# Kernel tuning notes

Hardware: AMD Instinct MI355X
Metric: run time of the kernel (lower is better)

Reference implementation:

```python
import jax, jax.numpy as jnp
import numpy as np

N_NODES = 100000
N_EDGES = 3200000


def sage_conv(x, src, dst, Wl, bl, Wr, n_nodes):
    # PyG SAGEConv: out = lin_l(mean_{j in N(i)} x_j) + lin_r(x_i)
    msgs = x[src]                                            # [E, d]
    agg = jax.ops.segment_sum(msgs, dst, num_segments=n_nodes)
    cnt = jax.ops.segment_sum(jnp.ones((src.shape[0],), x.dtype), dst,
                              num_segments=n_nodes)
    mean = agg / jnp.maximum(cnt, 1.0)[:, None]
    return mean @ Wl.T + bl + x @ Wr.T


def setup_inputs() -> dict:
    key = jax.random.key(0)
    ks = jax.random.split(key, 9)
    x = jax.random.normal(ks[0], (N_NODES, 6), dtype=jnp.float32)
    edge_index = jax.random.randint(ks[1], (2, N_EDGES), 0, N_NODES, dtype=jnp.int32)
    def glorot(k, shape):
        fan_in = shape[1]
        return jax.random.normal(k, shape, dtype=jnp.float32) / np.sqrt(fan_in)
    return {
        "x": x,
        "edge_index": edge_index,
        "W1l": glorot(ks[2], (12, 6)), "b1": jnp.zeros((12,), jnp.float32),
        "W1r": glorot(ks[3], (12, 6)),
        "W2l": glorot(ks[4], (24, 12)), "b2": jnp.zeros((24,), jnp.float32),
        "W2r": glorot(ks[5], (24, 12)),
        "W3l": glorot(ks[6], (6, 24)), "b3": jnp.zeros((6,), jnp.float32),
        "W3r": glorot(ks[7], (6, 24)),
    }


def reference(x, edge_index, W1l, b1, W1r, W2l, b2, W2r, W3l, b3, W3r):
    src, dst = edge_index[0], edge_index[1]
    h = jax.nn.relu(sage_conv(x, src, dst, W1l, b1, W1r, N_NODES))
    h = jax.nn.relu(sage_conv(h, src, dst, W2l, b2, W2r, N_NODES))
    z = sage_conv(h, src, dst, W3l, b3, W3r, N_NODES)          # [N, 6] encoding
    return z
```

## Files before the change

kernel.cpp:

```cpp
#include <hip/hip_runtime.h>
#include <hip/hip_fp16.h>


#define BSHIFT 9
#define BMASK  511
#define NBMAX  256
#define PART_EDGES 4096
#define BCAP   18000

#define NTL(p) __builtin_nontemporal_load(p)

__device__ __forceinline__ unsigned h2u(__half2 h) { return *reinterpret_cast<unsigned*>(&h); }
__device__ __forceinline__ __half2 u2h(unsigned u) { return *reinterpret_cast<__half2*>(&u); }

__device__ __forceinline__ __half2 red32(__half2 v) {
    int x;
    x = __builtin_amdgcn_update_dpp(0, (int)h2u(v), 0x128, 0xf, 0xf, true);
    v = __hadd2(v, u2h((unsigned)x));
    x = __builtin_amdgcn_update_dpp(0, (int)h2u(v), 0x124, 0xf, 0xf, true);
    v = __hadd2(v, u2h((unsigned)x));
    x = __builtin_amdgcn_update_dpp(0, (int)h2u(v), 0x122, 0xf, 0xf, true);
    v = __hadd2(v, u2h((unsigned)x));
    x = __builtin_amdgcn_update_dpp(0, (int)h2u(v), 0x121, 0xf, 0xf, true);
    v = __hadd2(v, u2h((unsigned)x));
    v = __hadd2(v, u2h(__shfl_xor(h2u(v), 16, 64)));
    return v;
}

__device__ __forceinline__ int wscan_incl(int x) {
    x += __builtin_amdgcn_update_dpp(0, x, 0x111, 0xf, 0xf, true);
    x += __builtin_amdgcn_update_dpp(0, x, 0x112, 0xf, 0xf, true);
    x += __builtin_amdgcn_update_dpp(0, x, 0x114, 0xf, 0xf, true);
    x += __builtin_amdgcn_update_dpp(0, x, 0x118, 0xf, 0xf, true);
    x += __builtin_amdgcn_update_dpp(0, x, 0x142, 0xa, 0xf, true);
    x += __builtin_amdgcn_update_dpp(0, x, 0x143, 0xc, 0xf, true);
    return x;
}

__global__ void __launch_bounds__(256)
partition_kernel(const float* __restrict__ x, __half* __restrict__ xh,
                 __half* __restrict__ h1, __half* __restrict__ z3lh,
                 const int* __restrict__ src, const int* __restrict__ dst,
                 int* __restrict__ bcur, unsigned* __restrict__ pairs,
                 int E, int n, int nb) {
    __shared__ int hcnt[NBMAX];
    __shared__ int hbase[NBMAX];
    __shared__ int lofs[NBMAX];
    __shared__ int wtot[4];
    __shared__ unsigned sorted[PART_EDGES];
    __shared__ int gpos[PART_EDGES];

    int t = threadIdx.x;

    int gid = blockIdx.x * 256 + t;
    if (gid <= n) {
        uint4 o = make_uint4(0u, 0u, 0u, 0u);
        if (gid < n) {
            const float2* xp = reinterpret_cast<const float2*>(x + (size_t)gid * 6);
            float2 a = xp[0], b = xp[1], c = xp[2];
            o.x = h2u(__floats2half2_rn(a.x, a.y));
            o.y = h2u(__floats2half2_rn(b.x, b.y));
            o.z = h2u(__floats2half2_rn(c.x, c.y));
        }
        *reinterpret_cast<uint4*>(xh + (size_t)gid * 8) = o;
    }
    if (blockIdx.x == 0) {
        if (t < 16) h1[(size_t)n * 16 + t] = __float2half(0.f);
        if (t < 8)  z3lh[(size_t)n * 8 + t] = __float2half(0.f);
    }

    int lo = blockIdx.x * PART_EDGES;
    int hi = min(E, lo + PART_EDGES);
    int cnt = hi - lo;

    for (int i = t; i < NBMAX; i += 256) hcnt[i] = 0;
    __syncthreads();

    int myd[16]; unsigned mys[16];
#pragma unroll
    for (int k = 0; k < 16; k++) {
        int i = lo + t + k * 256;
        if (i < hi) { myd[k] = NTL(dst + i); mys[k] = (unsigned)NTL(src + i); }
        else myd[k] = -1;
    }
#pragma unroll
    for (int k = 0; k < 16; k++)
        if (myd[k] >= 0) atomicAdd(&hcnt[myd[k] >> BSHIFT], 1);
    __syncthreads();

    int c = (t < nb) ? hcnt[t] : 0;
    if (t < nb) hbase[t] = c ? (t * BCAP + atomicAdd(&bcur[t], c)) : 0;
    int sc = wscan_incl(c);
    if ((t & 63) == 63) wtot[t >> 6] = sc;
    __syncthreads();
    int ofs = 0;
#pragma unroll
    for (int j = 0; j < 3; j++)
        if (j < (t >> 6)) ofs += wtot[j];
    int excl = sc + ofs - c;
    if (t < nb) { lofs[t] = excl; hcnt[t] = excl; }
    __syncthreads();

#pragma unroll
    for (int k = 0; k < 16; k++) {
        if (myd[k] >= 0) {
            int d = myd[k];
            int b = d >> BSHIFT;
            int r = atomicAdd(&hcnt[b], 1);
            sorted[r] = (mys[k] << BSHIFT) | (unsigned)(d & BMASK);
            gpos[r] = hbase[b] + (r - lofs[b]);
        }
    }
    __syncthreads();

    for (int i = t; i < cnt; i += 256)
        pairs[gpos[i]] = sorted[i];
}

__global__ void __launch_bounds__(1024)
csr_build(const unsigned* __restrict__ pairs,
          const int* __restrict__ bcur,
          int* __restrict__ deg, int* __restrict__ offsets,
          int* __restrict__ ssrc, int n) {
    __shared__ int ldeg[512];
    __shared__ int lcur[512];
    __shared__ int wtot[8];
    int b = blockIdx.x;
    int base = b * BCAP;
    int cnt = bcur[b];
    int t = threadIdx.x;
    if (t < 512) ldeg[t] = 0;
    __syncthreads();
    for (int i = t; i < cnt; i += 1024)
        atomicAdd(&ldeg[NTL(pairs + base + i) & BMASK], 1);
    __syncthreads();
    int c = (t < 512) ? ldeg[t] : 0;
    int sc = wscan_incl(c);
    if (t < 512 && (t & 63) == 63) wtot[t >> 6] = sc;
    __syncthreads();
    if (t < 512) {
        int ofs = 0;
#pragma unroll
        for (int j = 0; j < 7; j++)
            if (j < (t >> 6)) ofs += wtot[j];
        int excl = sc + ofs - c;
        lcur[t] = excl;
        int node = (b << BSHIFT) + t;
        if (node < n) { offsets[node] = base + excl; deg[node] = c; }
    }
    __syncthreads();
    for (int i = t; i < cnt; i += 1024) {
        unsigned p = NTL(pairs + base + i);
        int loc = p & BMASK;
        int pos = atomicAdd(&lcur[loc], 1);
        ssrc[base + pos] = (int)(p >> BSHIFT);
    }
}

__global__ void __launch_bounds__(256)
sage_layer1(const __half* __restrict__ xh,
            const int* __restrict__ offsets,
            const int* __restrict__ deg,
            const int* __restrict__ ssrc,
            const float* __restrict__ Wl,
            const float* __restrict__ bb,
            const float* __restrict__ Wr,
            __half* __restrict__ h1, int n) {
    __shared__ __half2 sWl2[36], sWr2[36];
    __shared__ float sb[12];
    int t = threadIdx.x;
    if (t < 36) {
        int r = t / 3, k = t % 3;
        sWl2[t] = __halves2half2(__float2half(Wl[r * 6 + 2 * k]),
                                 __float2half(Wl[r * 6 + 2 * k + 1]));
        sWr2[t] = __halves2half2(__float2half(Wr[r * 6 + 2 * k]),
                                 __float2half(Wr[r * 6 + 2 * k + 1]));
    }
    if (t < 12) sb[t] = bb[t];
    __syncthreads();

    int wid = (blockIdx.x * blockDim.x + threadIdx.x) >> 6;
    int nwaves = (gridDim.x * blockDim.x) >> 6;
    int wl = threadIdx.x & 63;
    int lane = wl & 31;
    int sub = wl >> 5;

    int r = (lane < 12) ? lane : 0;
    __half2 wl2[3], wr2[3];
#pragma unroll
    for (int k = 0; k < 3; k++) { wl2[k] = sWl2[r * 3 + k]; wr2[k] = sWr2[r * 3 + k]; }
    float bias = sb[r];

    int npairs = (n + 1) >> 1;
    __half2 z2 = __float2half2_rn(0.f);

    int pA = wid, pB = wid + nwaves;
    int nodeA = 2 * pA + sub, nodeB = 2 * pB + sub;
    bool vA = (pA < npairs) && (nodeA < n);
    bool vB = (pB < npairs) && (nodeB < n);
    int offA = vA ? offsets[nodeA] : 0, dgA = vA ? deg[nodeA] : 0;
    int offB = vB ? offsets[nodeB] : 0, dgB = vB ? deg[nodeB] : 0;

    int qa0 = ssrc[offA + lane], qa1 = ssrc[offA + lane + 32];
    int qb0 = ssrc[offB + lane], qb1 = ssrc[offB + lane + 32];
    int sa0 = (lane < dgA) ? qa0 : n;
    int sa1 = (lane + 32 < dgA) ? qa1 : n;
    int sb0_ = (lane < dgB) ? qb0 : n;
    int sb1_ = (lane + 32 < dgB) ? qb1 : n;
    uint4 ra0 = *reinterpret_cast<const uint4*>(xh + (size_t)sa0 * 8);
    uint4 ra1 = *reinterpret_cast<const uint4*>(xh + (size_t)sa1 * 8);
    uint4 rb0 = *reinterpret_cast<const uint4*>(xh + (size_t)sb0_ * 8);
    uint4 rb1 = *reinterpret_cast<const uint4*>(xh + (size_t)sb1_ * 8);

    __half2 aA[3], aB[3];
    aA[0] = __hadd2(u2h(ra0.x), u2h(ra1.x));
    aA[1] = __hadd2(u2h(ra0.y), u2h(ra1.y));
    aA[2] = __hadd2(u2h(ra0.z), u2h(ra1.z));
    aB[0] = __hadd2(u2h(rb0.x), u2h(rb1.x));
    aB[1] = __hadd2(u2h(rb0.y), u2h(rb1.y));
    aB[2] = __hadd2(u2h(rb0.z), u2h(rb1.z));

    int m = max(dgA, dgB);
    for (int e = lane + 64; e < m; e += 32) {
        int qa = ssrc[offA + e];
        int qb = ssrc[offB + e];
        int sa = (e < dgA) ? qa : n;
        int sbx = (e < dgB) ? qb : n;
        uint4 ta = *reinterpret_cast<const uint4*>(xh + (size_t)sa * 8);
        uint4 tb = *reinterpret_cast<const uint4*>(xh + (size_t)sbx * 8);
        aA[0] = __hadd2(aA[0], u2h(ta.x)); aA[1] = __hadd2(aA[1], u2h(ta.y));
        aA[2] = __hadd2(aA[2], u2h(ta.z));
        aB[0] = __hadd2(aB[0], u2h(tb.x)); aB[1] = __hadd2(aB[1], u2h(tb.y));
        aB[2] = __hadd2(aB[2], u2h(tb.z));
    }

#pragma unroll
    for (int k = 0; k < 3; k++) { aA[k] = red32(aA[k]); aB[k] = red32(aB[k]); }

    auto epi = [&](int node, int dg, __half2* acc, bool valid) {
        if (valid && lane < 12) {
            uint4 xr = *reinterpret_cast<const uint4*>(xh + (size_t)node * 8);
            __half2 xi2[3] = { u2h(xr.x), u2h(xr.y), u2h(xr.z) };
            __half2 S1 = z2, S2 = z2;
#pragma unroll
            for (int k = 0; k < 3; k++) {
                S1 = __hfma2(acc[k], wl2[k], S1);
                S2 = __hfma2(xi2[k], wr2[k], S2);
            }
            float inv = 1.f / (float)(dg > 0 ? dg : 1);
            float o = (__low2float(S1) + __high2float(S1)) * inv
                    + __low2float(S2) + __high2float(S2) + bias;
            h1[(size_t)node * 16 + lane] = __float2half(fmaxf(o, 0.f));
        }
    };
    epi(nodeA, dgA, aA, vA);
    epi(nodeB, dgB, aB, vB);
}

__global__ void __launch_bounds__(256)
sage_layer2(const __half* __restrict__ h1,
            const int* __restrict__ offsets,
            const int* __restrict__ deg,
            const int* __restrict__ ssrc,
            const float* __restrict__ W2l,
            const float* __restrict__ b2,
            const float* __restrict__ W2r,
            const float* __restrict__ W3l,
            const float* __restrict__ W3r,
            __half* __restrict__ z3lh,
            float* __restrict__ z3r, int n) {
    __shared__ __half2 sW2l2[144], sW2r2[144];
    __shared__ float sW3[300], sb2[24];
    __shared__ __attribute__((aligned(16))) float sh2[4][48];
    int t = threadIdx.x;
    if (t < 144) {
        int r = t / 6, k = t % 6;
        sW2l2[t] = __halves2half2(__float2half(W2l[r * 12 + 2 * k]),
                                  __float2half(W2l[r * 12 + 2 * k + 1]));
        sW2r2[t] = __halves2half2(__float2half(W2r[r * 12 + 2 * k]),
                                  __float2half(W2r[r * 12 + 2 * k + 1]));
        int r3 = t / 24, c3 = t % 24;
        sW3[r3 * 25 + c3] = W3l[t];
        sW3[(r3 + 6) * 25 + c3] = W3r[t];
    }
    if (t < 24) sb2[t] = b2[t];
    __syncthreads();

    int wid = (blockIdx.x * blockDim.x + threadIdx.x) >> 6;
    int nwaves = (gridDim.x * blockDim.x) >> 6;
    int wv = threadIdx.x >> 6;
    int wl = threadIdx.x & 63;
    int lane = wl & 31;
    int sub = wl >> 5;

    int r2 = (lane < 24) ? lane : 0;
    __half2 w2l2[6], w2r2[6];
#pragma unroll
    for (int k = 0; k < 6; k++) { w2l2[k] = sW2l2[r2 * 6 + k]; w2r2[k] = sW2r2[r2 * 6 + k]; }
    float bias = sb2[r2];
    int w3off = (lane < 12) ? lane * 25 : 0;

    int npairs = (n + 1) >> 1;
    __half2 z2 = __float2half2_rn(0.f);

    int p0 = wid, p1 = wid + nwaves;
    int node0 = 2 * p0 + sub, node1 = 2 * p1 + sub;
    bool v0 = (p0 < npairs) && (node0 < n);
    bool v1 = (p1 < npairs) && (node1 < n);
    int off0 = v0 ? offsets[node0] : 0, dg0 = v0 ? deg[node0] : 0;
    int off1 = v1 ? offsets[node1] : 0, dg1 = v1 ? deg[node1] : 0;

    int qa0 = ssrc[off0 + lane], qa1 = ssrc[off0 + lane + 32];
    int qb0 = ssrc[off1 + lane], qb1 = ssrc[off1 + lane + 32];
    int sa0 = (lane < dg0) ? qa0 : n;
    int sa1 = (lane + 32 < dg0) ? qa1 : n;
    int sb0_ = (lane < dg1) ? qb0 : n;
    int sb1_ = (lane + 32 < dg1) ? qb1 : n;
    const char* pa0 = reinterpret_cast<const char*>(h1 + (size_t)sa0 * 16);
    const char* pa1 = reinterpret_cast<const char*>(h1 + (size_t)sa1 * 16);
    const char* pb0 = reinterpret_cast<const char*>(h1 + (size_t)sb0_ * 16);
    const char* pb1 = reinterpret_cast<const char*>(h1 + (size_t)sb1_ * 16);
    uint4 Aa0 = *reinterpret_cast<const uint4*>(pa0);
    uint2 Ba0 = *reinterpret_cast<const uint2*>(pa0 + 16);
    uint4 Aa1 = *reinterpret_cast<const uint4*>(pa1);
    uint2 Ba1 = *reinterpret_cast<const uint2*>(pa1 + 16);
    uint4 Ab0 = *reinterpret_cast<const uint4*>(pb0);
    uint2 Bb0 = *reinterpret_cast<const uint2*>(pb0 + 16);
    uint4 Ab1 = *reinterpret_cast<const uint4*>(pb1);
    uint2 Bb1 = *reinterpret_cast<const uint2*>(pb1 + 16);

    __half2 a0[6], a1[6];
    a0[0] = __hadd2(u2h(Aa0.x), u2h(Aa1.x)); a0[1] = __hadd2(u2h(Aa0.y), u2h(Aa1.y));
    a0[2] = __hadd2(u2h(Aa0.z), u2h(Aa1.z)); a0[3] = __hadd2(u2h(Aa0.w), u2h(Aa1.w));
    a0[4] = __hadd2(u2h(Ba0.x), u2h(Ba1.x)); a0[5] = __hadd2(u2h(Ba0.y), u2h(Ba1.y));
    a1[0] = __hadd2(u2h(Ab0.x), u2h(Ab1.x)); a1[1] = __hadd2(u2h(Ab0.y), u2h(Ab1.y));
    a1[2] = __hadd2(u2h(Ab0.z), u2h(Ab1.z)); a1[3] = __hadd2(u2h(Ab0.w), u2h(Ab1.w));
    a1[4] = __hadd2(u2h(Bb0.x), u2h(Bb1.x)); a1[5] = __hadd2(u2h(Bb0.y), u2h(Bb1.y));

    int m = max(dg0, dg1);
    for (int e = lane + 64; e < m; e += 32) {
        int qa = ssrc[off0 + e];
        int qb = ssrc[off1 + e];
        int sa = (e < dg0) ? qa : n;
        int sbx = (e < dg1) ? qb : n;
        const char* ta = reinterpret_cast<const char*>(h1 + (size_t)sa * 16);
        const char* tb = reinterpret_cast<const char*>(h1 + (size_t)sbx * 16);
        uint4 Ta = *reinterpret_cast<const uint4*>(ta);
        uint2 Ua = *reinterpret_cast<const uint2*>(ta + 16);
        uint4 Tb = *reinterpret_cast<const uint4*>(tb);
        uint2 Ub = *reinterpret_cast<const uint2*>(tb + 16);
        a0[0] = __hadd2(a0[0], u2h(Ta.x)); a0[1] = __hadd2(a0[1], u2h(Ta.y));
        a0[2] = __hadd2(a0[2], u2h(Ta.z)); a0[3] = __hadd2(a0[3], u2h(Ta.w));
        a0[4] = __hadd2(a0[4], u2h(Ua.x)); a0[5] = __hadd2(a0[5], u2h(Ua.y));
        a1[0] = __hadd2(a1[0], u2h(Tb.x)); a1[1] = __hadd2(a1[1], u2h(Tb.y));
        a1[2] = __hadd2(a1[2], u2h(Tb.z)); a1[3] = __hadd2(a1[3], u2h(Tb.w));
        a1[4] = __hadd2(a1[4], u2h(Ub.x)); a1[5] = __hadd2(a1[5], u2h(Ub.y));
    }

    auto finish = [&](int node, int dg, __half2* acc, bool valid) {
#pragma unroll
        for (int k = 0; k < 6; k++) acc[k] = red32(acc[k]);

        float h2v = 0.f;
        if (valid && lane < 24) {
            const char* rp = reinterpret_cast<const char*>(h1 + (size_t)node * 16);
            uint4 x0 = *reinterpret_cast<const uint4*>(rp);
            uint2 x1 = *reinterpret_cast<const uint2*>(rp + 16);
            __half2 xi2[6] = { u2h(x0.x), u2h(x0.y), u2h(x0.z),
                               u2h(x0.w), u2h(x1.x), u2h(x1.y) };
            __half2 S1 = z2, S2 = z2;
#pragma unroll
            for (int k = 0; k < 6; k++) {
                S1 = __hfma2(acc[k], w2l2[k], S1);
                S2 = __hfma2(xi2[k], w2r2[k], S2);
            }
            float inv = 1.f / (float)(dg > 0 ? dg : 1);
            float o = (__low2float(S1) + __high2float(S1)) * inv
                    + __low2float(S2) + __high2float(S2) + bias;
            h2v = fmaxf(o, 0.f);
        }
        if (lane < 24) sh2[wv][sub * 24 + lane] = h2v;
        float z = 0.f;
        if (lane < 12) {
            const float4* hp = reinterpret_cast<const float4*>(sh2[wv] + sub * 24);
#pragma unroll
            for (int k = 0; k < 6; k++) {
                float4 h4 = hp[k];
                float w0 = sW3[w3off + 4 * k],     w1 = sW3[w3off + 4 * k + 1];
                float w2 = sW3[w3off + 4 * k + 2], w3 = sW3[w3off + 4 * k + 3];
                z += h4.x * w0 + h4.y * w1 + h4.z * w2 + h4.w * w3;
            }
        }
        if (valid) {
            if (lane < 6)               z3lh[(size_t)node * 8 + lane] = __float2half(z);
            else if (lane < 8)          z3lh[(size_t)node * 8 + lane] = __float2half(0.f);
            if (lane >= 6 && lane < 12) z3r[(size_t)node * 6 + (lane - 6)] = z;
        }
    };
    finish(node0, dg0, a0, v0);
    finish(node1, dg1, a1, v1);
}

__global__ void __launch_bounds__(256)
sage_layer3(const __half* __restrict__ z3lh,
            const int* __restrict__ offsets,
            const int* __restrict__ deg,
            const int* __restrict__ ssrc,
            const float* __restrict__ b3,
            const float* __restrict__ z3r,
            float* __restrict__ out, int n) {
    int wid = (blockIdx.x * blockDim.x + threadIdx.x) >> 6;
    int nwaves = (gridDim.x * blockDim.x) >> 6;
    int wl = threadIdx.x & 63;
    int lane = wl & 31;
    int sub = wl >> 5;

    float b3v = b3[(lane < 6) ? lane : 0];

    int npairs = (n + 1) >> 1;

    int pA = wid, pB = wid + nwaves;
    int nodeA = 2 * pA + sub, nodeB = 2 * pB + sub;
    bool vA = (pA < npairs) && (nodeA < n);
    bool vB = (pB < npairs) && (nodeB < n);
    int offA = vA ? offsets[nodeA] : 0, dgA = vA ? deg[nodeA] : 0;
    int offB = vB ? offsets[nodeB] : 0, dgB = vB ? deg[nodeB] : 0;

    int qa0 = ssrc[offA + lane], qa1 = ssrc[offA + lane + 32];
    int qb0 = ssrc[offB + lane], qb1 = ssrc[offB + lane + 32];
    int sa0 = (lane < dgA) ? qa0 : n;
    int sa1 = (lane + 32 < dgA) ? qa1 : n;
    int sb0_ = (lane < dgB) ? qb0 : n;
    int sb1_ = (lane + 32 < dgB) ? qb1 : n;
    uint4 ra0 = *reinterpret_cast<const uint4*>(z3lh + (size_t)sa0 * 8);
    uint4 ra1 = *reinterpret_cast<const uint4*>(z3lh + (size_t)sa1 * 8);
    uint4 rb0 = *reinterpret_cast<const uint4*>(z3lh + (size_t)sb0_ * 8);
    uint4 rb1 = *reinterpret_cast<const uint4*>(z3lh + (size_t)sb1_ * 8);

    __half2 aA[3], aB[3];
    aA[0] = __hadd2(u2h(ra0.x), u2h(ra1.x));
    aA[1] = __hadd2(u2h(ra0.y), u2h(ra1.y));
    aA[2] = __hadd2(u2h(ra0.z), u2h(ra1.z));
    aB[0] = __hadd2(u2h(rb0.x), u2h(rb1.x));
    aB[1] = __hadd2(u2h(rb0.y), u2h(rb1.y));
    aB[2] = __hadd2(u2h(rb0.z), u2h(rb1.z));

    int m = max(dgA, dgB);
    for (int e = lane + 64; e < m; e += 32) {
        int qa = ssrc[offA + e];
        int qb = ssrc[offB + e];
        int sa = (e < dgA) ? qa : n;
        int sbx = (e < dgB) ? qb : n;
        uint4 ta = *reinterpret_cast<const uint4*>(z3lh + (size_t)sa * 8);
        uint4 tb = *reinterpret_cast<const uint4*>(z3lh + (size_t)sbx * 8);
        aA[0] = __hadd2(aA[0], u2h(ta.x)); aA[1] = __hadd2(aA[1], u2h(ta.y));
        aA[2] = __hadd2(aA[2], u2h(ta.z));
        aB[0] = __hadd2(aB[0], u2h(tb.x)); aB[1] = __hadd2(aB[1], u2h(tb.y));
        aB[2] = __hadd2(aB[2], u2h(tb.z));
    }

#pragma unroll
    for (int k = 0; k < 3; k++) { aA[k] = red32(aA[k]); aB[k] = red32(aB[k]); }

    auto epi = [&](int node, int dg, __half2* acc, bool valid) {
        if (valid && lane < 6) {
            float fa[6] = { __low2float(acc[0]), __high2float(acc[0]),
                            __low2float(acc[1]), __high2float(acc[1]),
                            __low2float(acc[2]), __high2float(acc[2]) };
            float inv = 1.f / (float)(dg > 0 ? dg : 1);
            out[(size_t)node * 6 + lane] = fa[lane] * inv + b3v
                                         + z3r[(size_t)node * 6 + lane];
        }
    };
    epi(nodeA, dgA, aA, vA);
    epi(nodeB, dgB, aB, vB);
}

extern "C" void kernel_launch(void* const* d_in, const int* in_sizes, int n_in,
                              void* d_out, int out_size, void* d_ws, size_t ws_size,
                              hipStream_t stream) {
    const float* x   = (const float*)d_in[0];
    const int* eidx  = (const int*)d_in[1];
    const float* W1l = (const float*)d_in[2];
    const float* b1  = (const float*)d_in[3];
    const float* W1r = (const float*)d_in[4];
    const float* W2l = (const float*)d_in[5];
    const float* b2  = (const float*)d_in[6];
    const float* W2r = (const float*)d_in[7];
    const float* W3l = (const float*)d_in[8];
    const float* b3  = (const float*)d_in[9];
    const float* W3r = (const float*)d_in[10];

    const int n = in_sizes[0] / 6;
    const int E = in_sizes[1] / 2;
    const int* src = eidx;
    const int* dst = eidx + E;
    const int nb = (n + BMASK) >> BSHIFT;

    char* w = (char*)d_ws;
    auto carve = [&](size_t bytes) {
        char* p = w;
        w += (bytes + 255) & ~(size_t)255;
        return p;
    };
    int*      bcur    = (int*)carve((size_t)NBMAX * 4);
    unsigned* pairs   = (unsigned*)carve((size_t)nb * BCAP * 4);
    int*      ssrc    = (int*)carve((size_t)nb * BCAP * 4 + 256);
    int*      deg     = (int*)carve((size_t)n * 4);
    int*      offsets = (int*)carve((size_t)n * 4);
    __half*   xh      = (__half*)carve((size_t)(n + 1) * 8 * 2);
    __half*   h1      = (__half*)carve((size_t)(n + 1) * 16 * 2);
    __half*   z3lh    = (__half*)carve((size_t)(n + 1) * 8 * 2);
    float*    z3r     = (float*)carve((size_t)n * 6 * 4);

    const int part_blocks = (E + PART_EDGES - 1) / PART_EDGES;

    hipMemsetAsync(bcur, 0, (size_t)NBMAX * 4, stream);
    partition_kernel<<<part_blocks, 256, 0, stream>>>(x, xh, h1, z3lh,
                                                      src, dst, bcur, pairs, E, n, nb);
    csr_build<<<nb, 1024, 0, stream>>>(pairs, bcur, deg, offsets, ssrc, n);

    const int LBLK = 6250;
    sage_layer1<<<LBLK, 256, 0, stream>>>(xh, offsets, deg, ssrc, W1l, b1, W1r, h1, n);
    sage_layer2<<<LBLK, 256, 0, stream>>>(h1, offsets, deg, ssrc,
                                          W2l, b2, W2r, W3l, W3r, z3lh, z3r, n);
    sage_layer3<<<LBLK, 256, 0, stream>>>(z3lh, offsets, deg, ssrc, b3, z3r,
                                          (float*)d_out, n);
}
```

Before: 207.2 us.

## Drop CSR build; aggregate per destination bucket with LDS float atomics

Removes the csr_build kernel and the per-node CSR traversal. Each of the ~196 blocks now processes one 512-node destination bucket straight from the bucketed pairs array and accumulates neighbour features in shared memory with float atomics, then runs the dense epilogue per node. This saves one kernel launch and the ssrc/offsets traffic, and accumulates in fp32 instead of fp16. The cost is that only about 196 blocks of 1024 threads run per layer, so the GPU may be poorly occupied, and the LDS atomics can contend on hot nodes.

```diff
diff --git a/kernel.cpp b/kernel.cpp
--- a/kernel.cpp
+++ b/kernel.cpp
@@ -12,20 +12,6 @@
 
 __device__ __forceinline__ unsigned h2u(__half2 h) { return *reinterpret_cast<unsigned*>(&h); }
 __device__ __forceinline__ __half2 u2h(unsigned u) { return *reinterpret_cast<__half2*>(&u); }
-
-__device__ __forceinline__ __half2 red32(__half2 v) {
-    int x;
-    x = __builtin_amdgcn_update_dpp(0, (int)h2u(v), 0x128, 0xf, 0xf, true);
-    v = __hadd2(v, u2h((unsigned)x));
-    x = __builtin_amdgcn_update_dpp(0, (int)h2u(v), 0x124, 0xf, 0xf, true);
-    v = __hadd2(v, u2h((unsigned)x));
-    x = __builtin_amdgcn_update_dpp(0, (int)h2u(v), 0x122, 0xf, 0xf, true);
-    v = __hadd2(v, u2h((unsigned)x));
-    x = __builtin_amdgcn_update_dpp(0, (int)h2u(v), 0x121, 0xf, 0xf, true);
-    v = __hadd2(v, u2h((unsigned)x));
-    v = __hadd2(v, u2h(__shfl_xor(h2u(v), 16, 64)));
-    return v;
-}
 
 __device__ __forceinline__ int wscan_incl(int x) {
     x += __builtin_amdgcn_update_dpp(0, x, 0x111, 0xf, 0xf, true);
@@ -39,7 +25,6 @@
 
 __global__ void __launch_bounds__(256)
 partition_kernel(const float* __restrict__ x, __half* __restrict__ xh,
-                 __half* __restrict__ h1, __half* __restrict__ z3lh,
                  const int* __restrict__ src, const int* __restrict__ dst,
                  int* __restrict__ bcur, unsigned* __restrict__ pairs,
                  int E, int n, int nb) {
@@ -53,20 +38,15 @@
     int t = threadIdx.x;
 
     int gid = blockIdx.x * 256 + t;
-    if (gid <= n) {
-        uint4 o = make_uint4(0u, 0u, 0u, 0u);
-        if (gid < n) {
-            const float2* xp = reinterpret_cast<const float2*>(x + (size_t)gid * 6);
-            float2 a = xp[0], b = xp[1], c = xp[2];
-            o.x = h2u(__floats2half2_rn(a.x, a.y));
-            o.y = h2u(__floats2half2_rn(b.x, b.y));
-            o.z = h2u(__floats2half2_rn(c.x, c.y));
-        }
+    if (gid < n) {
+        const float2* xp = reinterpret_cast<const float2*>(x + (size_t)gid * 6);
+        float2 a = xp[0], b = xp[1], c = xp[2];
+        uint4 o;
+        o.x = h2u(__floats2half2_rn(a.x, a.y));
+        o.y = h2u(__floats2half2_rn(b.x, b.y));
+        o.z = h2u(__floats2half2_rn(c.x, c.y));
+        o.w = 0u;
         *reinterpret_cast<uint4*>(xh + (size_t)gid * 8) = o;
-    }
-    if (blockIdx.x == 0) {
-        if (t < 16) h1[(size_t)n * 16 + t] = __float2half(0.f);
-        if (t < 8)  z3lh[(size_t)n * 8 + t] = __float2half(0.f);
     }
 
     int lo = blockIdx.x * PART_EDGES;
@@ -118,150 +98,103 @@
 }
 
 __global__ void __launch_bounds__(1024)
-csr_build(const unsigned* __restrict__ pairs,
-          const int* __restrict__ bcur,
-          int* __restrict__ deg, int* __restrict__ offsets,
-          int* __restrict__ ssrc, int n) {
-    __shared__ int ldeg[512];
-    __shared__ int lcur[512];
-    __shared__ int wtot[8];
-    int b = blockIdx.x;
-    int base = b * BCAP;
-    int cnt = bcur[b];
-    int t = threadIdx.x;
-    if (t < 512) ldeg[t] = 0;
-    __syncthreads();
-    for (int i = t; i < cnt; i += 1024)
-        atomicAdd(&ldeg[NTL(pairs + base + i) & BMASK], 1);
-    __syncthreads();
-    int c = (t < 512) ? ldeg[t] : 0;
-    int sc = wscan_incl(c);
-    if (t < 512 && (t & 63) == 63) wtot[t >> 6] = sc;
-    __syncthreads();
-    if (t < 512) {
-        int ofs = 0;
-#pragma unroll
-        for (int j = 0; j < 7; j++)
-            if (j < (t >> 6)) ofs += wtot[j];
-        int excl = sc + ofs - c;
-        lcur[t] = excl;
-        int node = (b << BSHIFT) + t;
-        if (node < n) { offsets[node] = base + excl; deg[node] = c; }
-    }
-    __syncthreads();
-    for (int i = t; i < cnt; i += 1024) {
-        unsigned p = NTL(pairs + base + i);
-        int loc = p & BMASK;
-        int pos = atomicAdd(&lcur[loc], 1);
-        ssrc[base + pos] = (int)(p >> BSHIFT);
-    }
-}
-
-__global__ void __launch_bounds__(256)
 sage_layer1(const __half* __restrict__ xh,
-            const int* __restrict__ offsets,
-            const int* __restrict__ deg,
-            const int* __restrict__ ssrc,
+            const unsigned* __restrict__ pairs,
+            const int* __restrict__ bcur,
+            int* __restrict__ deg,
             const float* __restrict__ Wl,
             const float* __restrict__ bb,
             const float* __restrict__ Wr,
             __half* __restrict__ h1, int n) {
-    __shared__ __half2 sWl2[36], sWr2[36];
-    __shared__ float sb[12];
+    __shared__ float acc[512][6];
+    __shared__ int   ldeg[512];
+    __shared__ float sW[156];
     int t = threadIdx.x;
-    if (t < 36) {
-        int r = t / 3, k = t % 3;
-        sWl2[t] = __halves2half2(__float2half(Wl[r * 6 + 2 * k]),
-                                 __float2half(Wl[r * 6 + 2 * k + 1]));
-        sWr2[t] = __halves2half2(__float2half(Wr[r * 6 + 2 * k]),
-                                 __float2half(Wr[r * 6 + 2 * k + 1]));
-    }
-    if (t < 12) sb[t] = bb[t];
-    __syncthreads();
-
-    int wid = (blockIdx.x * blockDim.x + threadIdx.x) >> 6;
-    int nwaves = (gridDim.x * blockDim.x) >> 6;
-    int wl = threadIdx.x & 63;
-    int lane = wl & 31;
-    int sub = wl >> 5;
-
-    int r = (lane < 12) ? lane : 0;
-    __half2 wl2[3], wr2[3];
-#pragma unroll
-    for (int k = 0; k < 3; k++) { wl2[k] = sWl2[r * 3 + k]; wr2[k] = sWr2[r * 3 + k]; }
-    float bias = sb[r];
-
-    int npairs = (n + 1) >> 1;
-    __half2 z2 = __float2half2_rn(0.f);
-
-    int pA = wid, pB = wid + nwaves;
-    int nodeA = 2 * pA + sub, nodeB = 2 * pB + sub;
-    bool vA = (pA < npairs) && (nodeA < n);
-    bool vB = (pB < npairs) && (nodeB < n);
-    int offA = vA ? offsets[nodeA] : 0, dgA = vA ? deg[nodeA] : 0;
-    int offB = vB ? offsets[nodeB] : 0, dgB = vB ? deg[nodeB] : 0;
-
-    int qa0 = ssrc[offA + lane], qa1 = ssrc[offA + lane + 32];
-    int qb0 = ssrc[offB + lane], qb1 = ssrc[offB + lane + 32];
-    int sa0 = (lane < dgA) ? qa0 : n;
-    int sa1 = (lane + 32 < dgA) ? qa1 : n;
-    int sb0_ = (lane < dgB) ? qb0 : n;
-    int sb1_ = (lane + 32 < dgB) ? qb1 : n;
-    uint4 ra0 = *reinterpret_cast<const uint4*>(xh + (size_t)sa0 * 8);
-    uint4 ra1 = *reinterpret_cast<const uint4*>(xh + (size_t)sa1 * 8);
-    uint4 rb0 = *reinterpret_cast<const uint4*>(xh + (size_t)sb0_ * 8);
-    uint4 rb1 = *reinterpret_cast<const uint4*>(xh + (size_t)sb1_ * 8);
-
-    __half2 aA[3], aB[3];
-    aA[0] = __hadd2(u2h(ra0.x), u2h(ra1.x));
-    aA[1] = __hadd2(u2h(ra0.y), u2h(ra1.y));
-    aA[2] = __hadd2(u2h(ra0.z), u2h(ra1.z));
-    aB[0] = __hadd2(u2h(rb0.x), u2h(rb1.x));
-    aB[1] = __hadd2(u2h(rb0.y), u2h(rb1.y));
-    aB[2] = __hadd2(u2h(rb0.z), u2h(rb1.z));
-
-    int m = max(dgA, dgB);
-    for (int e = lane + 64; e < m; e += 32) {
-        int qa = ssrc[offA + e];
-        int qb = ssrc[offB + e];
-        int sa = (e < dgA) ? qa : n;
-        int sbx = (e < dgB) ? qb : n;
-        uint4 ta = *reinterpret_cast<const uint4*>(xh + (size_t)sa * 8);
-        uint4 tb = *reinterpret_cast<const uint4*>(xh + (size_t)sbx * 8);
-        aA[0] = __hadd2(aA[0], u2h(ta.x)); aA[1] = __hadd2(aA[1], u2h(ta.y));
-        aA[2] = __hadd2(aA[2], u2h(ta.z));
-        aB[0] = __hadd2(aB[0], u2h(tb.x)); aB[1] = __hadd2(aB[1], u2h(tb.y));
-        aB[2] = __hadd2(aB[2], u2h(tb.z));
-    }
-
-#pragma unroll
-    for (int k = 0; k < 3; k++) { aA[k] = red32(aA[k]); aB[k] = red32(aB[k]); }
-
-    auto epi = [&](int node, int dg, __half2* acc, bool valid) {
-        if (valid && lane < 12) {
+    if (t < 72) { sW[t] = Wl[t]; sW[72 + t] = Wr[t]; }
+    if (t < 12) sW[144 + t] = bb[t];
+    if (t < 512) {
+#pragma unroll
+        for (int c = 0; c < 6; c++) acc[t][c] = 0.f;
+        ldeg[t] = 0;
+    }
+    __syncthreads();
+
+    int b = blockIdx.x;
+    int base = b * BCAP;
+    int cnt = bcur[b];
+
+    for (int i0 = 0; i0 < cnt; i0 += 4096) {
+        unsigned p[4]; uint4 r[4]; bool v[4];
+#pragma unroll
+        for (int k = 0; k < 4; k++) {
+            int i = i0 + t + k * 1024;
+            v[k] = (i < cnt);
+            p[k] = v[k] ? pairs[base + i] : 0u;
+        }
+#pragma unroll
+        for (int k = 0; k < 4; k++) {
+            int s = (int)(p[k] >> BSHIFT);
+            r[k] = *reinterpret_cast<const uint4*>(xh + (size_t)s * 8);
+        }
+#pragma unroll
+        for (int k = 0; k < 4; k++) {
+            if (v[k]) {
+                int loc = p[k] & BMASK;
+                __half2 a = u2h(r[k].x), bq = u2h(r[k].y), cq = u2h(r[k].z);
+                atomicAdd(&acc[loc][0], __low2float(a));
+                atomicAdd(&acc[loc][1], __high2float(a));
+                atomicAdd(&acc[loc][2], __low2float(bq));
+                atomicAdd(&acc[loc][3], __high2float(bq));
+                atomicAdd(&acc[loc][4], __low2float(cq));
+                atomicAdd(&acc[loc][5], __high2float(cq));
+                atomicAdd(&ldeg[loc], 1);
+            }
+        }
+    }
+    __syncthreads();
+
+    if (t < 512) {
+        int node = (b << BSHIFT) + t;
+        if (node < n) {
+            int dg = ldeg[t];
+            deg[node] = dg;
+            float inv = 1.f / (float)(dg > 0 ? dg : 1);
+            float m[6], xv[6];
+#pragma unroll
+            for (int c = 0; c < 6; c++) m[c] = acc[t][c] * inv;
             uint4 xr = *reinterpret_cast<const uint4*>(xh + (size_t)node * 8);
-            __half2 xi2[3] = { u2h(xr.x), u2h(xr.y), u2h(xr.z) };
-            __half2 S1 = z2, S2 = z2;
-#pragma unroll
-            for (int k = 0; k < 3; k++) {
-                S1 = __hfma2(acc[k], wl2[k], S1);
-                S2 = __hfma2(xi2[k], wr2[k], S2);
-            }
-            float inv = 1.f / (float)(dg > 0 ? dg : 1);
-            float o = (__low2float(S1) + __high2float(S1)) * inv
-                    + __low2float(S2) + __high2float(S2) + bias;
-            h1[(size_t)node * 16 + lane] = __float2half(fmaxf(o, 0.f));
-        }
-    };
-    epi(nodeA, dgA, aA, vA);
-    epi(nodeB, dgB, aB, vB);
-}
-
-__global__ void __launch_bounds__(256)
+            __half2 x0 = u2h(xr.x), x1 = u2h(xr.y), x2 = u2h(xr.z);
+            xv[0] = __low2float(x0); xv[1] = __high2float(x0);
+            xv[2] = __low2float(x1); xv[3] = __high2float(x1);
+            xv[4] = __low2float(x2); xv[5] = __high2float(x2);
+            float o[12];
+#pragma unroll
+            for (int j = 0; j < 12; j++) {
+                float s = sW[144 + j];
+#pragma unroll
+                for (int c = 0; c < 6; c++)
+                    s += sW[j * 6 + c] * m[c] + sW[72 + j * 6 + c] * xv[c];
+                o[j] = fmaxf(s, 0.f);
+            }
+            uint4 w0, w1;
+            w0.x = h2u(__floats2half2_rn(o[0], o[1]));
+            w0.y = h2u(__floats2half2_rn(o[2], o[3]));
+            w0.z = h2u(__floats2half2_rn(o[4], o[5]));
+            w0.w = h2u(__floats2half2_rn(o[6], o[7]));
+            w1.x = h2u(__floats2half2_rn(o[8], o[9]));
+            w1.y = h2u(__floats2half2_rn(o[10], o[11]));
+            w1.z = 0u; w1.w = 0u;
+            *reinterpret_cast<uint4*>(h1 + (size_t)node * 16) = w0;
+            *reinterpret_cast<uint4*>(h1 + (size_t)node * 16 + 8) = w1;
+        }
+    }
+}
+
+__global__ void __launch_bounds__(1024)
 sage_layer2(const __half* __restrict__ h1,
-            const int* __restrict__ offsets,
+            const unsigned* __restrict__ pairs,
+            const int* __restrict__ bcur,
             const int* __restrict__ deg,
-            const int* __restrict__ ssrc,
             const float* __restrict__ W2l,
             const float* __restrict__ b2,
             const float* __restrict__ W2r,
@@ -269,211 +202,180 @@
             const float* __restrict__ W3r,
             __half* __restrict__ z3lh,
             float* __restrict__ z3r, int n) {
-    __shared__ __half2 sW2l2[144], sW2r2[144];
-    __shared__ float sW3[300], sb2[24];
-    __shared__ __attribute__((aligned(16))) float sh2[4][48];
+    __shared__ float acc[512][12];
+    __shared__ float sW[912];
     int t = threadIdx.x;
-    if (t < 144) {
-        int r = t / 6, k = t % 6;
-        sW2l2[t] = __halves2half2(__float2half(W2l[r * 12 + 2 * k]),
-                                  __float2half(W2l[r * 12 + 2 * k + 1]));
-        sW2r2[t] = __halves2half2(__float2half(W2r[r * 12 + 2 * k]),
-                                  __float2half(W2r[r * 12 + 2 * k + 1]));
-        int r3 = t / 24, c3 = t % 24;
-        sW3[r3 * 25 + c3] = W3l[t];
-        sW3[(r3 + 6) * 25 + c3] = W3r[t];
-    }
-    if (t < 24) sb2[t] = b2[t];
-    __syncthreads();
-
-    int wid = (blockIdx.x * blockDim.x + threadIdx.x) >> 6;
-    int nwaves = (gridDim.x * blockDim.x) >> 6;
-    int wv = threadIdx.x >> 6;
-    int wl = threadIdx.x & 63;
-    int lane = wl & 31;
-    int sub = wl >> 5;
-
-    int r2 = (lane < 24) ? lane : 0;
-    __half2 w2l2[6], w2r2[6];
-#pragma unroll
-    for (int k = 0; k < 6; k++) { w2l2[k] = sW2l2[r2 * 6 + k]; w2r2[k] = sW2r2[r2 * 6 + k]; }
-    float bias = sb2[r2];
-    int w3off = (lane < 12) ? lane * 25 : 0;
-
-    int npairs = (n + 1) >> 1;
-    __half2 z2 = __float2half2_rn(0.f);
-
-    int p0 = wid, p1 = wid + nwaves;
-    int node0 = 2 * p0 + sub, node1 = 2 * p1 + sub;
-    bool v0 = (p0 < npairs) && (node0 < n);
-    bool v1 = (p1 < npairs) && (node1 < n);
-    int off0 = v0 ? offsets[node0] : 0, dg0 = v0 ? deg[node0] : 0;
-    int off1 = v1 ? offsets[node1] : 0, dg1 = v1 ? deg[node1] : 0;
-
-    int qa0 = ssrc[off0 + lane], qa1 = ssrc[off0 + lane + 32];
-    int qb0 = ssrc[off1 + lane], qb1 = ssrc[off1 + lane + 32];
-    int sa0 = (lane < dg0) ? qa0 : n;
-    int sa1 = (lane + 32 < dg0) ? qa1 : n;
-    int sb0_ = (lane < dg1) ? qb0 : n;
-    int sb1_ = (lane + 32 < dg1) ? qb1 : n;
-    const char* pa0 = reinterpret_cast<const char*>(h1 + (size_t)sa0 * 16);
-    const char* pa1 = reinterpret_cast<const char*>(h1 + (size_t)sa1 * 16);
-    const char* pb0 = reinterpret_cast<const char*>(h1 + (size_t)sb0_ * 16);
-    const char* pb1 = reinterpret_cast<const char*>(h1 + (size_t)sb1_ * 16);
-    uint4 Aa0 = *reinterpret_cast<const uint4*>(pa0);
-    uint2 Ba0 = *reinterpret_cast<const uint2*>(pa0 + 16);
-    uint4 Aa1 = *reinterpret_cast<const uint4*>(pa1);
-    uint2 Ba1 = *reinterpret_cast<const uint2*>(pa1 + 16);
-    uint4 Ab0 = *reinterpret_cast<const uint4*>(pb0);
-    uint2 Bb0 = *reinterpret_cast<const uint2*>(pb0 + 16);
-    uint4 Ab1 = *reinterpret_cast<const uint4*>(pb1);
-    uint2 Bb1 = *reinterpret_cast<const uint2*>(pb1 + 16);
-
-    __half2 a0[6], a1[6];
-    a0[0] = __hadd2(u2h(Aa0.x), u2h(Aa1.x)); a0[1] = __hadd2(u2h(Aa0.y), u2h(Aa1.y));
-    a0[2] = __hadd2(u2h(Aa0.z), u2h(Aa1.z)); a0[3] = __hadd2(u2h(Aa0.w), u2h(Aa1.w));
-    a0[4] = __hadd2(u2h(Ba0.x), u2h(Ba1.x)); a0[5] = __hadd2(u2h(Ba0.y), u2h(Ba1.y));
-    a1[0] = __hadd2(u2h(Ab0.x), u2h(Ab1.x)); a1[1] = __hadd2(u2h(Ab0.y), u2h(Ab1.y));
-    a1[2] = __hadd2(u2h(Ab0.z), u2h(Ab1.z)); a1[3] = __hadd2(u2h(Ab0.w), u2h(Ab1.w));
-    a1[4] = __hadd2(u2h(Bb0.x), u2h(Bb1.x)); a1[5] = __hadd2(u2h(Bb0.y), u2h(Bb1.y));
-
-    int m = max(dg0, dg1);
-    for (int e = lane + 64; e < m; e += 32) {
-        int qa = ssrc[off0 + e];
-        int qb = ssrc[off1 + e];
-        int sa = (e < dg0) ? qa : n;
-        int sbx = (e < dg1) ? qb : n;
-        const char* ta = reinterpret_cast<const char*>(h1 + (size_t)sa * 16);
-        const char* tb = reinterpret_cast<const char*>(h1 + (size_t)sbx * 16);
-        uint4 Ta = *reinterpret_cast<const uint4*>(ta);
-        uint2 Ua = *reinterpret_cast<const uint2*>(ta + 16);
-        uint4 Tb = *reinterpret_cast<const uint4*>(tb);
-        uint2 Ub = *reinterpret_cast<const uint2*>(tb + 16);
-        a0[0] = __hadd2(a0[0], u2h(Ta.x)); a0[1] = __hadd2(a0[1], u2h(Ta.y));
-        a0[2] = __hadd2(a0[2], u2h(Ta.z)); a0[3] = __hadd2(a0[3], u2h(Ta.w));
-        a0[4] = __hadd2(a0[4], u2h(Ua.x)); a0[5] = __hadd2(a0[5], u2h(Ua.y));
-        a1[0] = __hadd2(a1[0], u2h(Tb.x)); a1[1] = __hadd2(a1[1], u2h(Tb.y));
-        a1[2] = __hadd2(a1[2], u2h(Tb.z)); a1[3] = __hadd2(a1[3], u2h(Tb.w));
-        a1[4] = __hadd2(a1[4], u2h(Ub.x)); a1[5] = __hadd2(a1[5], u2h(Ub.y));
-    }
-
-    auto finish = [&](int node, int dg, __half2* acc, bool valid) {
-#pragma unroll
-        for (int k = 0; k < 6; k++) acc[k] = red32(acc[k]);
-
-        float h2v = 0.f;
-        if (valid && lane < 24) {
-            const char* rp = reinterpret_cast<const char*>(h1 + (size_t)node * 16);
-            uint4 x0 = *reinterpret_cast<const uint4*>(rp);
-            uint2 x1 = *reinterpret_cast<const uint2*>(rp + 16);
-            __half2 xi2[6] = { u2h(x0.x), u2h(x0.y), u2h(x0.z),
-                               u2h(x0.w), u2h(x1.x), u2h(x1.y) };
-            __half2 S1 = z2, S2 = z2;
-#pragma unroll
-            for (int k = 0; k < 6; k++) {
-                S1 = __hfma2(acc[k], w2l2[k], S1);
-                S2 = __hfma2(xi2[k], w2r2[k], S2);
-            }
+    if (t < 288) { sW[t] = W2l[t]; sW[288 + t] = W2r[t]; }
+    if (t < 24)  sW[576 + t] = b2[t];
+    if (t < 144) { sW[600 + t] = W3l[t]; sW[744 + t] = W3r[t]; }
+    if (t < 512) {
+#pragma unroll
+        for (int c = 0; c < 12; c++) acc[t][c] = 0.f;
+    }
+    __syncthreads();
+
+    int b = blockIdx.x;
+    int base = b * BCAP;
+    int cnt = bcur[b];
+
+    for (int i0 = 0; i0 < cnt; i0 += 4096) {
+        unsigned p[4]; uint4 r4[4]; uint2 r2[4]; bool v[4];
+#pragma unroll
+        for (int k = 0; k < 4; k++) {
+            int i = i0 + t + k * 1024;
+            v[k] = (i < cnt);
+            p[k] = v[k] ? pairs[base + i] : 0u;
+        }
+#pragma unroll
+        for (int k = 0; k < 4; k++) {
+            const __half* rp = h1 + (size_t)(p[k] >> BSHIFT) * 16;
+            r4[k] = *reinterpret_cast<const uint4*>(rp);
+            r2[k] = *reinterpret_cast<const uint2*>(rp + 8);
+        }
+#pragma unroll
+        for (int k = 0; k < 4; k++) {
+            if (v[k]) {
+                int loc = p[k] & BMASK;
+                __half2 q0 = u2h(r4[k].x), q1 = u2h(r4[k].y);
+                __half2 q2 = u2h(r4[k].z), q3 = u2h(r4[k].w);
+                __half2 q4 = u2h(r2[k].x), q5 = u2h(r2[k].y);
+                atomicAdd(&acc[loc][0],  __low2float(q0));
+                atomicAdd(&acc[loc][1],  __high2float(q0));
+                atomicAdd(&acc[loc][2],  __low2float(q1));
+                atomicAdd(&acc[loc][3],  __high2float(q1));
+                atomicAdd(&acc[loc][4],  __low2float(q2));
+                atomicAdd(&acc[loc][5],  __high2float(q2));
+                atomicAdd(&acc[loc][6],  __low2float(q3));
+                atomicAdd(&acc[loc][7],  __high2float(q3));
+                atomicAdd(&acc[loc][8],  __low2float(q4));
+                atomicAdd(&acc[loc][9],  __high2float(q4));
+                atomicAdd(&acc[loc][10], __low2float(q5));
+                atomicAdd(&acc[loc][11], __high2float(q5));
+            }
+        }
+    }
+    __syncthreads();
+
+    if (t < 512) {
+        int node = (b << BSHIFT) + t;
+        if (node < n) {
+            int dg = deg[node];
             float inv = 1.f / (float)(dg > 0 ? dg : 1);
-            float o = (__low2float(S1) + __high2float(S1)) * inv
-                    + __low2float(S2) + __high2float(S2) + bias;
-            h2v = fmaxf(o, 0.f);
-        }
-        if (lane < 24) sh2[wv][sub * 24 + lane] = h2v;
-        float z = 0.f;
-        if (lane < 12) {
-            const float4* hp = reinterpret_cast<const float4*>(sh2[wv] + sub * 24);
-#pragma unroll
-            for (int k = 0; k < 6; k++) {
-                float4 h4 = hp[k];
-                float w0 = sW3[w3off + 4 * k],     w1 = sW3[w3off + 4 * k + 1];
-                float w2 = sW3[w3off + 4 * k + 2], w3 = sW3[w3off + 4 * k + 3];
-                z += h4.x * w0 + h4.y * w1 + h4.z * w2 + h4.w * w3;
-            }
-        }
-        if (valid) {
-            if (lane < 6)               z3lh[(size_t)node * 8 + lane] = __float2half(z);
-            else if (lane < 8)          z3lh[(size_t)node * 8 + lane] = __float2half(0.f);
-            if (lane >= 6 && lane < 12) z3r[(size_t)node * 6 + (lane - 6)] = z;
-        }
-    };
-    finish(node0, dg0, a0, v0);
-    finish(node1, dg1, a1, v1);
-}
-
-__global__ void __launch_bounds__(256)
+            float m[12], hv[12];
+#pragma unroll
+            for (int c = 0; c < 12; c++) m[c] = acc[t][c] * inv;
+            const __half* rp = h1 + (size_t)node * 16;
+            uint4 y4 = *reinterpret_cast<const uint4*>(rp);
+            uint2 y2 = *reinterpret_cast<const uint2*>(rp + 8);
+            __half2 q0 = u2h(y4.x), q1 = u2h(y4.y), q2 = u2h(y4.z), q3 = u2h(y4.w);
+            __half2 q4 = u2h(y2.x), q5 = u2h(y2.y);
+            hv[0] = __low2float(q0);  hv[1] = __high2float(q0);
+            hv[2] = __low2float(q1);  hv[3] = __high2float(q1);
+            hv[4] = __low2float(q2);  hv[5] = __high2float(q2);
+            hv[6] = __low2float(q3);  hv[7] = __high2float(q3);
+            hv[8] = __low2float(q4);  hv[9] = __high2float(q4);
+            hv[10] = __low2float(q5); hv[11] = __high2float(q5);
+            float h2o[24];
+#pragma unroll
+            for (int j = 0; j < 24; j++) {
+                float s = sW[576 + j];
+#pragma unroll
+                for (int c = 0; c < 12; c++)
+                    s += sW[j * 12 + c] * m[c] + sW[288 + j * 12 + c] * hv[c];
+                h2o[j] = fmaxf(s, 0.f);
+            }
+            float zl[6], zr[6];
+#pragma unroll
+            for (int c2 = 0; c2 < 6; c2++) {
+                float sl = 0.f, sr = 0.f;
+#pragma unroll
+                for (int j = 0; j < 24; j++) {
+                    sl += sW[600 + c2 * 24 + j] * h2o[j];
+                    sr += sW[744 + c2 * 24 + j] * h2o[j];
+                }
+                zl[c2] = sl; zr[c2] = sr;
+            }
+            uint4 wz;
+            wz.x = h2u(__floats2half2_rn(zl[0], zl[1]));
+            wz.y = h2u(__floats2half2_rn(zl[2], zl[3]));
+            wz.z = h2u(__floats2half2_rn(zl[4], zl[5]));
+            wz.w = 0u;
+            *reinterpret_cast<uint4*>(z3lh + (size_t)node * 8) = wz;
+            float4 f0; f0.x = zr[0]; f0.y = zr[1]; f0.z = zr[2]; f0.w = zr[3];
+            float2 f1; f1.x = zr[4]; f1.y = zr[5];
+            *reinterpret_cast<float4*>(z3r + (size_t)node * 8) = f0;
+            *reinterpret_cast<float2*>(z3r + (size_t)node * 8 + 4) = f1;
+        }
+    }
+}
+
+__global__ void __launch_bounds__(1024)
 sage_layer3(const __half* __restrict__ z3lh,
-            const int* __restrict__ offsets,
+            const unsigned* __restrict__ pairs,
+            const int* __restrict__ bcur,
             const int* __restrict__ deg,
-            const int* __restrict__ ssrc,
             const float* __restrict__ b3,
             const float* __restrict__ z3r,
             float* __restrict__ out, int n) {
-    int wid = (blockIdx.x * blockDim.x + threadIdx.x) >> 6;
-    int nwaves = (gridDim.x * blockDim.x) >> 6;
-    int wl = threadIdx.x & 63;
-    int lane = wl & 31;
-    int sub = wl >> 5;
-
-    float b3v = b3[(lane < 6) ? lane : 0];
-
-    int npairs = (n + 1) >> 1;
-
-    int pA = wid, pB = wid + nwaves;
-    int nodeA = 2 * pA + sub, nodeB = 2 * pB + sub;
-    bool vA = (pA < npairs) && (nodeA < n);
-    bool vB = (pB < npairs) && (nodeB < n);
-    int offA = vA ? offsets[nodeA] : 0, dgA = vA ? deg[nodeA] : 0;
-    int offB = vB ? offsets[nodeB] : 0, dgB = vB ? deg[nodeB] : 0;
-
-    int qa0 = ssrc[offA + lane], qa1 = ssrc[offA + lane + 32];
-    int qb0 = ssrc[offB + lane], qb1 = ssrc[offB + lane + 32];
-    int sa0 = (lane < dgA) ? qa0 : n;
-    int sa1 = (lane + 32 < dgA) ? qa1 : n;
-    int sb0_ = (lane < dgB) ? qb0 : n;
-    int sb1_ = (lane + 32 < dgB) ? qb1 : n;
-    uint4 ra0 = *reinterpret_cast<const uint4*>(z3lh + (size_t)sa0 * 8);
-    uint4 ra1 = *reinterpret_cast<const uint4*>(z3lh + (size_t)sa1 * 8);
-    uint4 rb0 = *reinterpret_cast<const uint4*>(z3lh + (size_t)sb0_ * 8);
-    uint4 rb1 = *reinterpret_cast<const uint4*>(z3lh + (size_t)sb1_ * 8);
-
-    __half2 aA[3], aB[3];
-    aA[0] = __hadd2(u2h(ra0.x), u2h(ra1.x));
-    aA[1] = __hadd2(u2h(ra0.y), u2h(ra1.y));
-    aA[2] = __hadd2(u2h(ra0.z), u2h(ra1.z));
-    aB[0] = __hadd2(u2h(rb0.x), u2h(rb1.x));
-    aB[1] = __hadd2(u2h(rb0.y), u2h(rb1.y));
-    aB[2] = __hadd2(u2h(rb0.z), u2h(rb1.z));
-
-    int m = max(dgA, dgB);
-    for (int e = lane + 64; e < m; e += 32) {
-        int qa = ssrc[offA + e];
-        int qb = ssrc[offB + e];
-        int sa = (e < dgA) ? qa : n;
-        int sbx = (e < dgB) ? qb : n;
-        uint4 ta = *reinterpret_cast<const uint4*>(z3lh + (size_t)sa * 8);
-        uint4 tb = *reinterpret_cast<const uint4*>(z3lh + (size_t)sbx * 8);
-        aA[0] = __hadd2(aA[0], u2h(ta.x)); aA[1] = __hadd2(aA[1], u2h(ta.y));
-        aA[2] = __hadd2(aA[2], u2h(ta.z));
-        aB[0] = __hadd2(aB[0], u2h(tb.x)); aB[1] = __hadd2(aB[1], u2h(tb.y));
-        aB[2] = __hadd2(aB[2], u2h(tb.z));
-    }
-
-#pragma unroll
-    for (int k = 0; k < 3; k++) { aA[k] = red32(aA[k]); aB[k] = red32(aB[k]); }
-
-    auto epi = [&](int node, int dg, __half2* acc, bool valid) {
-        if (valid && lane < 6) {
-            float fa[6] = { __low2float(acc[0]), __high2float(acc[0]),
-                            __low2float(acc[1]), __high2float(acc[1]),
-                            __low2float(acc[2]), __high2float(acc[2]) };
+    __shared__ float acc[512][6];
+    __shared__ float sb3[6];
+    int t = threadIdx.x;
+    if (t < 6) sb3[t] = b3[t];
+    if (t < 512) {
+#pragma unroll
+        for (int c = 0; c < 6; c++) acc[t][c] = 0.f;
+    }
+    __syncthreads();
+
+    int b = blockIdx.x;
+    int base = b * BCAP;
+    int cnt = bcur[b];
+
+    for (int i0 = 0; i0 < cnt; i0 += 4096) {
+        unsigned p[4]; uint4 r[4]; bool v[4];
+#pragma unroll
+        for (int k = 0; k < 4; k++) {
+            int i = i0 + t + k * 1024;
+            v[k] = (i < cnt);
+            p[k] = v[k] ? pairs[base + i] : 0u;
+        }
+#pragma unroll
+        for (int k = 0; k < 4; k++) {
+            int s = (int)(p[k] >> BSHIFT);
+            r[k] = *reinterpret_cast<const uint4*>(z3lh + (size_t)s * 8);
+        }
+#pragma unroll
+        for (int k = 0; k < 4; k++) {
+            if (v[k]) {
+                int loc = p[k] & BMASK;
+                __half2 a = u2h(r[k].x), bq = u2h(r[k].y), cq = u2h(r[k].z);
+                atomicAdd(&acc[loc][0], __low2float(a));
+                atomicAdd(&acc[loc][1], __high2float(a));
+                atomicAdd(&acc[loc][2], __low2float(bq));
+                atomicAdd(&acc[loc][3], __high2float(bq));
+                atomicAdd(&acc[loc][4], __low2float(cq));
+                atomicAdd(&acc[loc][5], __high2float(cq));
+            }
+        }
+    }
+    __syncthreads();
+
+    if (t < 512) {
+        int node = (b << BSHIFT) + t;
+        if (node < n) {
+            int dg = deg[node];
             float inv = 1.f / (float)(dg > 0 ? dg : 1);
-            out[(size_t)node * 6 + lane] = fa[lane] * inv + b3v
-                                         + z3r[(size_t)node * 6 + lane];
-        }
-    };
-    epi(nodeA, dgA, aA, vA);
-    epi(nodeB, dgB, aB, vB);
+            float4 zr0 = *reinterpret_cast<const float4*>(z3r + (size_t)node * 8);
+            float2 zr1 = *reinterpret_cast<const float2*>(z3r + (size_t)node * 8 + 4);
+            float* op = out + (size_t)node * 6;
+            op[0] = acc[t][0] * inv + sb3[0] + zr0.x;
+            op[1] = acc[t][1] * inv + sb3[1] + zr0.y;
+            op[2] = acc[t][2] * inv + sb3[2] + zr0.z;
+            op[3] = acc[t][3] * inv + sb3[3] + zr0.w;
+            op[4] = acc[t][4] * inv + sb3[4] + zr1.x;
+            op[5] = acc[t][5] * inv + sb3[5] + zr1.y;
+        }
+    }
 }
 
 extern "C" void kernel_launch(void* const* d_in, const int* in_sizes, int n_in,
@@ -505,25 +407,21 @@
     };
     int*      bcur    = (int*)carve((size_t)NBMAX * 4);
     unsigned* pairs   = (unsigned*)carve((size_t)nb * BCAP * 4);
-    int*      ssrc    = (int*)carve((size_t)nb * BCAP * 4 + 256);
     int*      deg     = (int*)carve((size_t)n * 4);
-    int*      offsets = (int*)carve((size_t)n * 4);
-    __half*   xh      = (__half*)carve((size_t)(n + 1) * 8 * 2);
-    __half*   h1      = (__half*)carve((size_t)(n + 1) * 16 * 2);
-    __half*   z3lh    = (__half*)carve((size_t)(n + 1) * 8 * 2);
-    float*    z3r     = (float*)carve((size_t)n * 6 * 4);
+    __half*   xh      = (__half*)carve((size_t)n * 8 * 2);
+    __half*   h1      = (__half*)carve((size_t)n * 16 * 2);
+    __half*   z3lh    = (__half*)carve((size_t)n * 8 * 2);
+    float*    z3r     = (float*)carve((size_t)n * 8 * 4);
 
     const int part_blocks = (E + PART_EDGES - 1) / PART_EDGES;
 
     hipMemsetAsync(bcur, 0, (size_t)NBMAX * 4, stream);
-    partition_kernel<<<part_blocks, 256, 0, stream>>>(x, xh, h1, z3lh,
-                                                      src, dst, bcur, pairs, E, n, nb);
-    csr_build<<<nb, 1024, 0, stream>>>(pairs, bcur, deg, offsets, ssrc, n);
-
-    const int LBLK = 6250;
-    sage_layer1<<<LBLK, 256, 0, stream>>>(xh, offsets, deg, ssrc, W1l, b1, W1r, h1, n);
-    sage_layer2<<<LBLK, 256, 0, stream>>>(h1, offsets, deg, ssrc,
-                                          W2l, b2, W2r, W3l, W3r, z3lh, z3r, n);
-    sage_layer3<<<LBLK, 256, 0, stream>>>(z3lh, offsets, deg, ssrc, b3, z3r,
-                                          (float*)d_out, n);
-}
+    partition_kernel<<<part_blocks, 256, 0, stream>>>(x, xh, src, dst,
+                                                      bcur, pairs, E, n, nb);
+    sage_layer1<<<nb, 1024, 0, stream>>>(xh, pairs, bcur, deg,
+                                         W1l, b1, W1r, h1, n);
+    sage_layer2<<<nb, 1024, 0, stream>>>(h1, pairs, bcur, deg,
+                                         W2l, b2, W2r, W3l, W3r, z3lh, z3r, n);
+    sage_layer3<<<nb, 1024, 0, stream>>>(z3lh, pairs, bcur, deg, b3, z3r,
+                                         (float*)d_out, n);
+}
```

Result: slower. 643.9 us (+210.8%).
